# Kernel tuning notes

Hardware: AMD Instinct MI355X
Metric: run time of the kernel (lower is better)

The kernel has to match this reference:

```python
import jax, jax.numpy as jnp
import numpy as np

B, S, D, H = 4, 2048, 1024, 16
HD = D // H  # head dim = 64


def setup_inputs() -> dict:
    key = jax.random.key(0)
    k1, k2, k3, k4, k5 = jax.random.split(key, 5)
    scale_qkv = 1.0 / np.sqrt(D)
    return {
        "x": jax.random.normal(k1, (B, S, D), dtype=jnp.float32),
        "w_qkv": jax.random.normal(k2, (D, 3 * D), dtype=jnp.float32) * scale_qkv,
        "b_qkv": jax.random.normal(k3, (3 * D,), dtype=jnp.float32) * 0.01,
        "w_out": jax.random.normal(k4, (D, D), dtype=jnp.float32) * scale_qkv,
        "b_out": jax.random.normal(k5, (D,), dtype=jnp.float32) * 0.01,
    }


def reference(x, w_qkv, b_qkv, w_out, b_out):
    b, s, d = x.shape
    qkv = (x @ w_qkv + b_qkv).reshape(b, s, 3, H, HD)
    qkv = jnp.transpose(qkv, (2, 0, 3, 1, 4))
    q, k, v = qkv[0], qkv[1], qkv[2]
    # scaled dot-product attention (materializes full [B,H,S,S] scores,
    # matching the original module)
    scores = jnp.einsum("bhqd,bhkd->bhqk", q, k) / jnp.sqrt(jnp.float32(HD))
    attn = jax.nn.softmax(scores, axis=-1)
    out = jnp.einsum("bhqk,bhkd->bhqd", attn, v)  # [B,H,S,HD]
    out = jnp.transpose(out, (0, 2, 1, 3)).reshape(b, s, d)
    return out @ w_out + b_out
```

## Files before the change

kernel.cpp:

```cpp
#include <hip/hip_runtime.h>
#include <stdint.h>

#define LOG2E 1.44269504088896340736f

typedef __attribute__((ext_vector_type(8))) __bf16 bf16x8;
typedef __attribute__((ext_vector_type(8))) short short8;
typedef __attribute__((ext_vector_type(4))) short s16x4;
typedef __attribute__((ext_vector_type(4))) float f32x4;

static __device__ __forceinline__ unsigned short f2bf(float f) {
    return __builtin_bit_cast(unsigned short, (__bf16)f);
}

static __device__ __forceinline__ float exp2_fast(float x) {
    float r;
    asm("v_exp_f32 %0, %1" : "=v"(r) : "v"(x));
    return r;
}

static __device__ __forceinline__ void gload_lds16(const void* g, void* l) {
    __builtin_amdgcn_global_load_lds(
        (const __attribute__((address_space(1))) unsigned int*)g,
        (__attribute__((address_space(3))) unsigned int*)l, 16, 0, 0);
}

static __device__ __forceinline__ int xcd_swz(int bid, int nwg) {
    return (bid & 7) * (nwg >> 3) + (bid >> 3);
}

__global__ __launch_bounds__(256) void k_cast_bf16(
    const float* __restrict__ x, unsigned short* __restrict__ xb)
{
    const int base = blockIdx.x * 2048;
    const float4* xin = (const float4*)(x + base);
    s16x4* xo = (s16x4*)(xb + base);
#pragma unroll
    for (int i = 0; i < 2; ++i) {
        const float4 f = xin[threadIdx.x + i * 256];
        s16x4 v;
        v[0] = (short)f2bf(f.x); v[1] = (short)f2bf(f.y);
        v[2] = (short)f2bf(f.z); v[3] = (short)f2bf(f.w);
        xo[threadIdx.x + i * 256] = v;
    }
}

__global__ __launch_bounds__(256) void k_transpose_bf16(
    const float* __restrict__ src, unsigned short* __restrict__ dst, int R, int C)
{
    __shared__ float t[32][33];
    const int tx = threadIdx.x, ty = threadIdx.y;
    const int c0 = blockIdx.x * 32, r0 = blockIdx.y * 32;
#pragma unroll
    for (int j = 0; j < 4; ++j)
        t[ty + j*8][tx] = src[(size_t)(r0 + ty + j*8) * C + (c0 + tx)];
    __syncthreads();
#pragma unroll
    for (int j = 0; j < 4; ++j)
        dst[(size_t)(c0 + ty + j*8) * R + (r0 + tx)] = f2bf(t[tx][ty + j*8]);
}

template <int NBN, int MODE>
__global__ __launch_bounds__(256) void k_gemm_bt(
    const unsigned short* __restrict__ A, const unsigned short* __restrict__ Bt,
    const float* __restrict__ bias,
    unsigned short* __restrict__ Qo, unsigned short* __restrict__ Ko,
    unsigned short* __restrict__ Vo, float* __restrict__ Co)
{
    constexpr int K = 1024;
    constexpr int NT = K / 32;
    constexpr int NN = NBN * 128;
    __shared__ __align__(16) short As[2][128 * 32];
    __shared__ __align__(16) short Bs[2][128 * 32];

    const int tid = threadIdx.x;
    const int w = tid >> 6, lane = tid & 63;
    const int lo16 = lane & 15, kg = lane >> 4;
    const int bid = xcd_swz(blockIdx.x, gridDim.x);
    const int bm = bid / NBN, bn = bid % NBN;
    const int wm = w >> 1, wn = w & 1;

    f32x4 acc[4][4] = {};

    const int c0 = w * 64 + lane, c1 = c0 + 256;
    const unsigned short* pA0 = A  + (size_t)(bm*128 + (c0 >> 2)) * K + (c0 & 3) * 8;
    const unsigned short* pA1 = A  + (size_t)(bm*128 + (c1 >> 2)) * K + (c1 & 3) * 8;
    const unsigned short* pB0 = Bt + (size_t)(bn*128 + (c0 >> 2)) * K + (c0 & 3) * 8;
    const unsigned short* pB1 = Bt + (size_t)(bn*128 + (c1 >> 2)) * K + (c1 & 3) * 8;

    auto STAGE = [&](int kt, int b) {
        gload_lds16(pA0 + kt*32, &As[b][w * 512]);
        gload_lds16(pA1 + kt*32, &As[b][(4 + w) * 512]);
        gload_lds16(pB0 + kt*32, &Bs[b][w * 512]);
        gload_lds16(pB1 + kt*32, &Bs[b][(4 + w) * 512]);
    };
    auto COMPUTE = [&](const short* Ab, const short* Bb) {
        bf16x8 af[4], bff[4];
#pragma unroll
        for (int rb = 0; rb < 4; ++rb)
            af[rb] = *(const bf16x8*)&Ab[(wm*64 + rb*16 + lo16) * 32 + kg*8];
#pragma unroll
        for (int cb = 0; cb < 4; ++cb)
            bff[cb] = *(const bf16x8*)&Bb[(wn*64 + cb*16 + lo16) * 32 + kg*8];
#pragma unroll
        for (int rb = 0; rb < 4; ++rb)
#pragma unroll
            for (int cb = 0; cb < 4; ++cb)
                acc[rb][cb] = __builtin_amdgcn_mfma_f32_16x16x32_bf16(af[rb], bff[cb], acc[rb][cb], 0, 0, 0);
    };

    STAGE(0, 0);
    __syncthreads();
    for (int kt = 0; kt < NT; kt += 2) {
        STAGE(kt + 1, 1);
        COMPUTE(As[0], Bs[0]);
        __syncthreads();
        if (kt + 2 < NT) STAGE(kt + 2, 0);
        COMPUTE(As[1], Bs[1]);
        __syncthreads();
    }

#pragma unroll
    for (int rb = 0; rb < 4; ++rb) {
        const int m0 = bm*128 + wm*64 + rb*16 + kg*4;
#pragma unroll
        for (int cb = 0; cb < 4; ++cb) {
            const int n = bn*128 + wn*64 + cb*16 + lo16;
            const float bv = bias[n];
            if constexpr (MODE == 0) {
                const int which = n >> 10;
                const int h = (n >> 6) & 15;
                const int hd = n & 63;
                if (which == 2) {
                    const int b = m0 >> 11, s0 = m0 & 2047;
                    const int head = b*16 + h;
                    unsigned long long pv = 0;
#pragma unroll
                    for (int r = 0; r < 4; ++r)
                        pv |= (unsigned long long)f2bf(acc[rb][cb][r] + bv) << (16*r);
                    *(unsigned long long*)(Vo + ((size_t)head*64 + hd)*2048 + s0) = pv;
                } else {
                    unsigned short* P = (which == 0) ? Qo : Ko;
                    const float scq = (which == 0) ? (0.125f * LOG2E) : 1.0f;
#pragma unroll
                    for (int r = 0; r < 4; ++r) {
                        const int m = m0 + r;
                        const int b = m >> 11, s = m & 2047;
                        P[((size_t)(b*16 + h)*2048 + s)*64 + hd] = f2bf((acc[rb][cb][r] + bv) * scq);
                    }
                }
            } else {
                (void)Qo; (void)Ko; (void)Vo;
#pragma unroll
                for (int r = 0; r < 4; ++r)
                    Co[(size_t)(m0 + r) * NN + n] = acc[rb][cb][r] + bv;
            }
        }
    }
}

__global__ __launch_bounds__(256, 4) void k_attn(
    const unsigned short* __restrict__ Qg, const unsigned short* __restrict__ Kg,
    const unsigned short* __restrict__ Vtg, unsigned short* __restrict__ Og)
{
    __shared__ __align__(16) short QP[128 * 64];
    __shared__ __align__(16) short Ks[2][64 * 64];
    __shared__ __align__(16) short Vs[2][64 * 64];

    const int tid = threadIdx.x;
    const int w = tid >> 6, lane = tid & 63;
    const int lo16 = lane & 15, kg = lane >> 4;
    const int head = blockIdx.x >> 4, qt = blockIdx.x & 15;
    const size_t hoff = (size_t)head * (2048 * 64);

    const int c0 = w*64 + lane, c1 = c0 + 256;
    const int r0 = c0 >> 3, j0 = (c0 & 7) ^ (r0 & 7);
    const int r1 = c1 >> 3, j1 = (c1 & 7) ^ (r1 & 7);
    const unsigned short* pK0 = Kg  + hoff + (size_t)r0*64 + j0*8;
    const unsigned short* pK1 = Kg  + hoff + (size_t)r1*64 + j1*8;
    const unsigned short* pV0 = Vtg + hoff + (size_t)r0*2048 + j0*8;
    const unsigned short* pV1 = Vtg + hoff + (size_t)r1*2048 + j1*8;

    auto STAGE = [&](int t, int b) {
        gload_lds16(pK0 + (size_t)t*4096, &Ks[b][w * 512]);
        gload_lds16(pK1 + (size_t)t*4096, &Ks[b][(4 + w) * 512]);
        gload_lds16(pV0 + t*64, &Vs[b][w * 512]);
        gload_lds16(pV1 + t*64, &Vs[b][(4 + w) * 512]);
    };

#pragma unroll
    for (int i = 0; i < 4; ++i) {
        const int c = (i*4 + w) * 64 + lane;
        const int row = c >> 3, j = (c & 7) ^ (row & 7);
        gload_lds16(Qg + hoff + (size_t)(qt*128 + row)*64 + j*8, &QP[(i*4 + w) * 512]);
    }
    STAGE(0, 0);
    __syncthreads();

    bf16x8 aq[2][2];
#pragma unroll
    for (int rb = 0; rb < 2; ++rb)
#pragma unroll
        for (int ks = 0; ks < 2; ++ks) {
            const int q = w*32 + rb*16 + lo16;
            const int blk = (ks*4 + kg) ^ (q & 7);
            aq[rb][ks] = *(const bf16x8*)&QP[q*64 + blk*8];
        }

    float m_run[2][4], l_run[2][4];
#pragma unroll
    for (int rb = 0; rb < 2; ++rb)
#pragma unroll
        for (int r = 0; r < 4; ++r) { m_run[rb][r] = -1e30f; l_run[rb][r] = 0.f; }
    f32x4 acc_o[2][4] = {};

    short* Pw = QP + w * 2048;

    auto COMPUTE = [&](const short* Kb, const short* Vb) {
        f32x4 sc[2][4] = {};
#pragma unroll
        for (int ks = 0; ks < 2; ++ks) {
            bf16x8 bk[4];
#pragma unroll
            for (int cb = 0; cb < 4; ++cb) {
                const int kv = cb*16 + lo16;
                const int blk = (ks*4 + kg) ^ (kv & 7);
                bk[cb] = *(const bf16x8*)&Kb[kv*64 + blk*8];
            }
#pragma unroll
            for (int rb = 0; rb < 2; ++rb)
#pragma unroll
                for (int cb = 0; cb < 4; ++cb)
                    sc[rb][cb] = __builtin_amdgcn_mfma_f32_16x16x32_bf16(aq[rb][ks], bk[cb], sc[rb][cb], 0, 0, 0);
        }

#pragma unroll
        for (int rb = 0; rb < 2; ++rb) {
#pragma unroll
            for (int r = 0; r < 4; ++r) {
                float t = fmaxf(fmaxf(sc[rb][0][r], sc[rb][1][r]),
                                fmaxf(sc[rb][2][r], sc[rb][3][r]));
                const float mo = m_run[rb][r];
                if (__any(t > mo + 8.0f)) {
                    t = fmaxf(t, __shfl_xor(t, 1));
                    t = fmaxf(t, __shfl_xor(t, 2));
                    t = fmaxf(t, __shfl_xor(t, 4));
                    t = fmaxf(t, __shfl_xor(t, 8));
                    const float mn = fmaxf(mo, t);
                    const float fac = exp2_fast(mo - mn);
                    m_run[rb][r] = mn;
                    l_run[rb][r] *= fac;
#pragma unroll
                    for (int hb = 0; hb < 4; ++hb) acc_o[rb][hb][r] *= fac;
                }
                const float m = m_run[rb][r];
                float s = 0.f;
#pragma unroll
                for (int cb = 0; cb < 4; ++cb) {
                    const float p = exp2_fast(sc[rb][cb][r] - m);
                    sc[rb][cb][r] = p;
                    s += p;
                }
                l_run[rb][r] += s;
            }
        }

#pragma unroll
        for (int rb = 0; rb < 2; ++rb)
#pragma unroll
            for (int cb = 0; cb < 4; ++cb)
#pragma unroll
                for (int r = 0; r < 4; ++r) {
                    const int q = rb*16 + kg*4 + r;
                    const int kv = cb*16 + lo16;
                    const int bo = q*128 + ((kv*2) ^ ((q & 7) << 4));
                    Pw[bo >> 1] = (short)f2bf(sc[rb][cb][r]);
                }

#pragma unroll
        for (int ks = 0; ks < 2; ++ks) {
            bf16x8 ap[2], bvv[4];
#pragma unroll
            for (int rb = 0; rb < 2; ++rb) {
                const int q = rb*16 + lo16;
                const int blk = (ks*4 + kg) ^ (q & 7);
                ap[rb] = *(const bf16x8*)&Pw[q*64 + blk*8];
            }
#pragma unroll
            for (int hb = 0; hb < 4; ++hb) {
                const int hd = hb*16 + lo16;
                const int blk = (ks*4 + kg) ^ (hd & 7);
                bvv[hb] = *(const bf16x8*)&Vb[hd*64 + blk*8];
            }
#pragma unroll
            for (int rb = 0; rb < 2; ++rb)
#pragma unroll
                for (int hb = 0; hb < 4; ++hb)
                    acc_o[rb][hb] = __builtin_amdgcn_mfma_f32_16x16x32_bf16(ap[rb], bvv[hb], acc_o[rb][hb], 0, 0, 0);
        }
    };

    for (int t = 0; t < 32; t += 2) {
        STAGE(t + 1, 1);
        COMPUTE(Ks[0], Vs[0]);
        __syncthreads();
        if (t + 2 < 32) STAGE(t + 2, 0);
        COMPUTE(Ks[1], Vs[1]);
        __syncthreads();
    }

    const int b = head >> 4, h = head & 15;
#pragma unroll
    for (int rb = 0; rb < 2; ++rb)
#pragma unroll
        for (int r = 0; r < 4; ++r) {
            float l = l_run[rb][r];
            l += __shfl_xor(l, 1);
            l += __shfl_xor(l, 2);
            l += __shfl_xor(l, 4);
            l += __shfl_xor(l, 8);
            const float inv = 1.0f / l;
            const int s = qt*128 + w*32 + rb*16 + kg*4 + r;
#pragma unroll
            for (int hb = 0; hb < 4; ++hb) {
                const int hd = hb*16 + lo16;
                Og[(size_t)(b*2048 + s)*1024 + h*64 + hd] = f2bf(acc_o[rb][hb][r] * inv);
            }
        }
}

extern "C" void kernel_launch(void* const* d_in, const int* in_sizes, int n_in,
                              void* d_out, int out_size, void* d_ws, size_t ws_size,
                              hipStream_t stream)
{
    const float* x      = (const float*)d_in[0];
    const float* w_qkv  = (const float*)d_in[1];
    const float* b_qkv  = (const float*)d_in[2];
    const float* w_out  = (const float*)d_in[3];
    const float* b_out  = (const float*)d_in[4];
    float* out = (float*)d_out;

    char* ws = (char*)d_ws;
    unsigned short* wqkv_t = (unsigned short*)(ws);
    unsigned short* wout_t = (unsigned short*)(ws +  6291456);
    unsigned short* Qb     = (unsigned short*)(ws +  8388608);
    unsigned short* Kb     = (unsigned short*)(ws + 25165824);
    unsigned short* Vb     = (unsigned short*)(ws + 41943040);
    unsigned short* AO     = (unsigned short*)(ws + 58720256);
    unsigned short* xb     = AO;

    k_cast_bf16<<<4096, 256, 0, stream>>>(x, xb);
    k_transpose_bf16<<<dim3(96, 32), dim3(32, 8), 0, stream>>>(w_qkv, wqkv_t, 1024, 3072);
    k_transpose_bf16<<<dim3(32, 32), dim3(32, 8), 0, stream>>>(w_out, wout_t, 1024, 1024);
    k_gemm_bt<24, 0><<<64 * 24, 256, 0, stream>>>(xb, wqkv_t, b_qkv, Qb, Kb, Vb, nullptr);
    k_attn<<<64 * 16, 256, 0, stream>>>(Qb, Kb, Vb, AO);
    k_gemm_bt<8, 1><<<64 * 8, 256, 0, stream>>>(AO, wout_t, b_out, nullptr, nullptr, nullptr, out);
}
```

Measured before the change: 339.7 us.

## Rework attention kernel to 32x32 MFMA with register-resident transposed P

Rewrites the flash-attention inner loop to compute S^T = K·Q^T with 32x32x16 MFMAs, so each lane owns one query column. The softmax row max and sum then reduce with a single cross-half shuffle. P stays in registers, packed with v_cvt_pk_bf16 and swapped between wave halves via shfl, instead of going through an LDS round-trip. Q fragments load directly from global into registers, which removes the Q/P shared buffer and cuts LDS use. The trade-offs are extra cross-lane bpermute traffic when rescaling and more complex lane mapping, which risks correctness and register-pressure problems.

```diff
diff --git a/kernel.cpp b/kernel.cpp
--- a/kernel.cpp
+++ b/kernel.cpp
@@ -7,6 +7,7 @@
 typedef __attribute__((ext_vector_type(8))) short short8;
 typedef __attribute__((ext_vector_type(4))) short s16x4;
 typedef __attribute__((ext_vector_type(4))) float f32x4;
+typedef __attribute__((ext_vector_type(16))) float f32x16;
 
 static __device__ __forceinline__ unsigned short f2bf(float f) {
     return __builtin_bit_cast(unsigned short, (__bf16)f);
@@ -162,141 +163,114 @@
     const unsigned short* __restrict__ Qg, const unsigned short* __restrict__ Kg,
     const unsigned short* __restrict__ Vtg, unsigned short* __restrict__ Og)
 {
-    __shared__ __align__(16) short QP[128 * 64];
     __shared__ __align__(16) short Ks[2][64 * 64];
     __shared__ __align__(16) short Vs[2][64 * 64];
 
     const int tid = threadIdx.x;
     const int w = tid >> 6, lane = tid & 63;
-    const int lo16 = lane & 15, kg = lane >> 4;
+    const int l31 = lane & 31, hi = lane >> 5, s7v = l31 & 7;
     const int head = blockIdx.x >> 4, qt = blockIdx.x & 15;
     const size_t hoff = (size_t)head * (2048 * 64);
 
-    const int c0 = w*64 + lane, c1 = c0 + 256;
+    const int c0 = w*64 + lane;
     const int r0 = c0 >> 3, j0 = (c0 & 7) ^ (r0 & 7);
-    const int r1 = c1 >> 3, j1 = (c1 & 7) ^ (r1 & 7);
     const unsigned short* pK0 = Kg  + hoff + (size_t)r0*64 + j0*8;
-    const unsigned short* pK1 = Kg  + hoff + (size_t)r1*64 + j1*8;
     const unsigned short* pV0 = Vtg + hoff + (size_t)r0*2048 + j0*8;
-    const unsigned short* pV1 = Vtg + hoff + (size_t)r1*2048 + j1*8;
 
     auto STAGE = [&](int t, int b) {
-        gload_lds16(pK0 + (size_t)t*4096, &Ks[b][w * 512]);
-        gload_lds16(pK1 + (size_t)t*4096, &Ks[b][(4 + w) * 512]);
-        gload_lds16(pV0 + t*64, &Vs[b][w * 512]);
-        gload_lds16(pV1 + t*64, &Vs[b][(4 + w) * 512]);
+        gload_lds16(pK0 + (size_t)t*4096,           &Ks[b][w * 512]);
+        gload_lds16(pK0 + (size_t)t*4096 + 32*64,   &Ks[b][(4 + w) * 512]);
+        gload_lds16(pV0 + t*64,                     &Vs[b][w * 512]);
+        gload_lds16(pV0 + t*64 + 32*2048,           &Vs[b][(4 + w) * 512]);
     };
 
-#pragma unroll
-    for (int i = 0; i < 4; ++i) {
-        const int c = (i*4 + w) * 64 + lane;
-        const int row = c >> 3, j = (c & 7) ^ (row & 7);
-        gload_lds16(Qg + hoff + (size_t)(qt*128 + row)*64 + j*8, &QP[(i*4 + w) * 512]);
-    }
+    bf16x8 qf[4];
+    {
+        const unsigned short* qrow = Qg + hoff + (size_t)(qt*128 + w*32 + l31) * 64;
+#pragma unroll
+        for (int kt = 0; kt < 4; ++kt)
+            qf[kt] = *(const bf16x8*)(qrow + kt*16 + hi*8);
+    }
+
     STAGE(0, 0);
     __syncthreads();
 
-    bf16x8 aq[2][2];
-#pragma unroll
-    for (int rb = 0; rb < 2; ++rb)
-#pragma unroll
-        for (int ks = 0; ks < 2; ++ks) {
-            const int q = w*32 + rb*16 + lo16;
-            const int blk = (ks*4 + kg) ^ (q & 7);
-            aq[rb][ks] = *(const bf16x8*)&QP[q*64 + blk*8];
-        }
-
-    float m_run[2][4], l_run[2][4];
-#pragma unroll
-    for (int rb = 0; rb < 2; ++rb)
-#pragma unroll
-        for (int r = 0; r < 4; ++r) { m_run[rb][r] = -1e30f; l_run[rb][r] = 0.f; }
-    f32x4 acc_o[2][4] = {};
-
-    short* Pw = QP + w * 2048;
+    float m_run = -1e30f, l_run = 0.f;
+    f32x16 ao0 = {}, ao1 = {};
 
     auto COMPUTE = [&](const short* Kb, const short* Vb) {
-        f32x4 sc[2][4] = {};
-#pragma unroll
-        for (int ks = 0; ks < 2; ++ks) {
-            bf16x8 bk[4];
-#pragma unroll
-            for (int cb = 0; cb < 4; ++cb) {
-                const int kv = cb*16 + lo16;
-                const int blk = (ks*4 + kg) ^ (kv & 7);
-                bk[cb] = *(const bf16x8*)&Kb[kv*64 + blk*8];
+        f32x16 s0 = {}, s1 = {};
+#pragma unroll
+        for (int kt = 0; kt < 4; ++kt) {
+            const int ch = (2*kt + hi) ^ s7v;
+            const bf16x8 k0 = *(const bf16x8*)&Kb[l31*64 + ch*8];
+            const bf16x8 k1 = *(const bf16x8*)&Kb[(32 + l31)*64 + ch*8];
+            s0 = __builtin_amdgcn_mfma_f32_32x32x16_bf16(k0, qf[kt], s0, 0, 0, 0);
+            s1 = __builtin_amdgcn_mfma_f32_32x32x16_bf16(k1, qf[kt], s1, 0, 0, 0);
+        }
+
+        float t = fmaxf(s0[0], s1[0]);
+#pragma unroll
+        for (int r = 1; r < 16; ++r) t = fmaxf(t, fmaxf(s0[r], s1[r]));
+        t = fmaxf(t, __shfl_xor(t, 32));
+        if (__any(t > m_run + 8.0f)) {
+            const float mn = fmaxf(m_run, t);
+            const float fac = exp2_fast(m_run - mn);
+            m_run = mn; l_run *= fac;
+            const int fi = __builtin_bit_cast(int, fac);
+#pragma unroll
+            for (int r = 0; r < 16; ++r) {
+                const int qa = (r & 3) + 8*(r >> 2) + 4*hi;
+                const float fr = __builtin_bit_cast(float,
+                    __builtin_amdgcn_ds_bpermute(qa << 2, fi));
+                ao0[r] *= fr; ao1[r] *= fr;
             }
-#pragma unroll
-            for (int rb = 0; rb < 2; ++rb)
-#pragma unroll
-                for (int cb = 0; cb < 4; ++cb)
-                    sc[rb][cb] = __builtin_amdgcn_mfma_f32_16x16x32_bf16(aq[rb][ks], bk[cb], sc[rb][cb], 0, 0, 0);
-        }
-
-#pragma unroll
-        for (int rb = 0; rb < 2; ++rb) {
-#pragma unroll
-            for (int r = 0; r < 4; ++r) {
-                float t = fmaxf(fmaxf(sc[rb][0][r], sc[rb][1][r]),
-                                fmaxf(sc[rb][2][r], sc[rb][3][r]));
-                const float mo = m_run[rb][r];
-                if (__any(t > mo + 8.0f)) {
-                    t = fmaxf(t, __shfl_xor(t, 1));
-                    t = fmaxf(t, __shfl_xor(t, 2));
-                    t = fmaxf(t, __shfl_xor(t, 4));
-                    t = fmaxf(t, __shfl_xor(t, 8));
-                    const float mn = fmaxf(mo, t);
-                    const float fac = exp2_fast(mo - mn);
-                    m_run[rb][r] = mn;
-                    l_run[rb][r] *= fac;
-#pragma unroll
-                    for (int hb = 0; hb < 4; ++hb) acc_o[rb][hb][r] *= fac;
-                }
-                const float m = m_run[rb][r];
-                float s = 0.f;
-#pragma unroll
-                for (int cb = 0; cb < 4; ++cb) {
-                    const float p = exp2_fast(sc[rb][cb][r] - m);
-                    sc[rb][cb][r] = p;
-                    s += p;
-                }
-                l_run[rb][r] += s;
+        }
+        float sum = 0.f;
+#pragma unroll
+        for (int r = 0; r < 16; ++r) {
+            const float p0 = exp2_fast(s0[r] - m_run); s0[r] = p0;
+            const float p1 = exp2_fast(s1[r] - m_run); s1[r] = p1;
+            sum += p0 + p1;
+        }
+        sum += __shfl_xor(sum, 32);
+        l_run += sum;
+
+        unsigned pk0[8], pk1[8];
+#pragma unroll
+        for (int m = 0; m < 4; ++m)
+#pragma unroll
+            for (int i = 0; i < 2; ++i) {
+                unsigned a, b2;
+                asm("v_cvt_pk_bf16_f32 %0, %1, %2"
+                    : "=v"(a) : "v"(s0[4*m + 2*i]), "v"(s0[4*m + 2*i + 1]));
+                asm("v_cvt_pk_bf16_f32 %0, %1, %2"
+                    : "=v"(b2) : "v"(s1[4*m + 2*i]), "v"(s1[4*m + 2*i + 1]));
+                pk0[m*2 + i] = a;
+                pk1[m*2 + i] = b2;
             }
-        }
-
-#pragma unroll
-        for (int rb = 0; rb < 2; ++rb)
-#pragma unroll
-            for (int cb = 0; cb < 4; ++cb)
-#pragma unroll
-                for (int r = 0; r < 4; ++r) {
-                    const int q = rb*16 + kg*4 + r;
-                    const int kv = cb*16 + lo16;
-                    const int bo = q*128 + ((kv*2) ^ ((q & 7) << 4));
-                    Pw[bo >> 1] = (short)f2bf(sc[rb][cb][r]);
-                }
-
-#pragma unroll
-        for (int ks = 0; ks < 2; ++ks) {
-            bf16x8 ap[2], bvv[4];
-#pragma unroll
-            for (int rb = 0; rb < 2; ++rb) {
-                const int q = rb*16 + lo16;
-                const int blk = (ks*4 + kg) ^ (q & 7);
-                ap[rb] = *(const bf16x8*)&Pw[q*64 + blk*8];
-            }
-#pragma unroll
-            for (int hb = 0; hb < 4; ++hb) {
-                const int hd = hb*16 + lo16;
-                const int blk = (ks*4 + kg) ^ (hd & 7);
-                bvv[hb] = *(const bf16x8*)&Vb[hd*64 + blk*8];
-            }
-#pragma unroll
-            for (int rb = 0; rb < 2; ++rb)
-#pragma unroll
-                for (int hb = 0; hb < 4; ++hb)
-                    acc_o[rb][hb] = __builtin_amdgcn_mfma_f32_16x16x32_bf16(ap[rb], bvv[hb], acc_o[rb][hb], 0, 0, 0);
-        }
+
+#define PV_STEP(KS, PK)                                                        \
+        {                                                                      \
+            constexpr int m0 = 2*((KS) & 1), m1 = m0 + 1;                      \
+            const unsigned snd0 = hi ? PK[m0*2+0] : PK[m1*2+0];                \
+            const unsigned snd1 = hi ? PK[m0*2+1] : PK[m1*2+1];                \
+            const unsigned rcv0 = (unsigned)__shfl_xor((int)snd0, 32);         \
+            const unsigned rcv1 = (unsigned)__shfl_xor((int)snd1, 32);         \
+            const unsigned kp0 = hi ? PK[m1*2+0] : PK[m0*2+0];                 \
+            const unsigned kp1 = hi ? PK[m1*2+1] : PK[m0*2+1];                 \
+            uint4 fw;                                                          \
+            fw.x = hi ? rcv0 : kp0;  fw.y = hi ? rcv1 : kp1;                   \
+            fw.z = hi ? kp0 : rcv0;  fw.w = hi ? kp1 : rcv1;                   \
+            const bf16x8 pa = __builtin_bit_cast(bf16x8, fw);                  \
+            const int ch = (2*(KS) + hi) ^ s7v;                                \
+            const bf16x8 v0 = *(const bf16x8*)&Vb[l31*64 + ch*8];              \
+            const bf16x8 v1 = *(const bf16x8*)&Vb[(32 + l31)*64 + ch*8];       \
+            ao0 = __builtin_amdgcn_mfma_f32_32x32x16_bf16(pa, v0, ao0, 0,0,0); \
+            ao1 = __builtin_amdgcn_mfma_f32_32x32x16_bf16(pa, v1, ao1, 0,0,0); \
+        }
+        PV_STEP(0, pk0) PV_STEP(1, pk0) PV_STEP(2, pk1) PV_STEP(3, pk1)
+#undef PV_STEP
     };
 
     for (int t = 0; t < 32; t += 2) {
@@ -309,23 +283,18 @@
     }
 
     const int b = head >> 4, h = head & 15;
-#pragma unroll
-    for (int rb = 0; rb < 2; ++rb)
-#pragma unroll
-        for (int r = 0; r < 4; ++r) {
-            float l = l_run[rb][r];
-            l += __shfl_xor(l, 1);
-            l += __shfl_xor(l, 2);
-            l += __shfl_xor(l, 4);
-            l += __shfl_xor(l, 8);
-            const float inv = 1.0f / l;
-            const int s = qt*128 + w*32 + rb*16 + kg*4 + r;
-#pragma unroll
-            for (int hb = 0; hb < 4; ++hb) {
-                const int hd = hb*16 + lo16;
-                Og[(size_t)(b*2048 + s)*1024 + h*64 + hd] = f2bf(acc_o[rb][hb][r] * inv);
-            }
-        }
+    const float inv = 1.0f / l_run;
+    const int ii = __builtin_bit_cast(int, inv);
+#pragma unroll
+    for (int r = 0; r < 16; ++r) {
+        const int qa = (r & 3) + 8*(r >> 2) + 4*hi;
+        const float vr = __builtin_bit_cast(float,
+            __builtin_amdgcn_ds_bpermute(qa << 2, ii));
+        const int s = qt*128 + w*32 + qa;
+        unsigned short* op = Og + (size_t)(b*2048 + s)*1024 + h*64;
+        op[l31]      = f2bf(ao0[r] * vr);
+        op[32 + l31] = f2bf(ao1[r] * vr);
+    }
 }
 
 extern "C" void kernel_launch(void* const* d_in, const int* in_sizes, int n_in,
```

After: 317.7 us. 6.5% less time.
